# Kernel tuning notes

Hardware: AMD Instinct MI355X
Metric: run time of the kernel (lower is better)

Reference implementation:

```python
import jax, jax.numpy as jnp
import numpy as np

EMBED_DIM = 1024
B, S = 8, 2048


def setup_inputs() -> dict:
    key = jax.random.key(0)
    ks = jax.random.split(key, 8)
    scale = 1.0 / np.sqrt(EMBED_DIM)
    return {
        "mha_output": jax.random.normal(ks[0], (B, S, EMBED_DIM), dtype=jnp.float32),
        "gates": jax.random.uniform(ks[1], (B, S), dtype=jnp.float32),
        "Wq": jax.random.uniform(ks[2], (EMBED_DIM, EMBED_DIM), jnp.float32, -scale, scale),
        "bq": jax.random.uniform(ks[3], (EMBED_DIM,), jnp.float32, -scale, scale),
        "Wk": jax.random.uniform(ks[4], (EMBED_DIM, EMBED_DIM), jnp.float32, -scale, scale),
        "bk": jax.random.uniform(ks[5], (EMBED_DIM,), jnp.float32, -scale, scale),
        "Wv": jax.random.uniform(ks[6], (EMBED_DIM, EMBED_DIM), jnp.float32, -scale, scale),
        "bv": jax.random.uniform(ks[7], (EMBED_DIM,), jnp.float32, -scale, scale),
    }


def reference(mha_output, gates, Wq, bq, Wk, bk, Wv, bv):
    # gates: (B, S) -> (B, S, 1) for elementwise modulation
    g = gates[..., None]
    # Linear layers (torch convention: x @ W^T + b)
    Q = jnp.einsum('bsd,ed->bse', mha_output, Wq) + bq
    K = jnp.einsum('bsd,ed->bse', mha_output, Wk) + bk
    V = jnp.einsum('bsd,ed->bse', mha_output, Wv) + bv
    Q_mod = Q * g
    K_mod = K * g
    temperature = jnp.sqrt(jnp.asarray(EMBED_DIM, dtype=mha_output.dtype))
    scores = jnp.einsum('bqd,bkd->bqk', Q_mod, K_mod) / temperature  # (B, S, S)
    attn_weights = jax.nn.softmax(scores, axis=-1)
    gated_attn_output = jnp.einsum('bqk,bkd->bqd', attn_weights, V)
    return gated_attn_output, attn_weights
```

## Files before the change

kernel.cpp:

```cpp
#include <hip/hip_runtime.h>

#define SEQ  2048
#define EMB  1024
#define NBAT 8
#define NROW (NBAT*SEQ)

using u16 = unsigned short;
typedef float  f32x4  __attribute__((ext_vector_type(4)));
typedef __bf16 bf16x8 __attribute__((ext_vector_type(8)));
typedef u16    u16x8  __attribute__((ext_vector_type(8)));
typedef u16    u16x4  __attribute__((ext_vector_type(4)));

__device__ __forceinline__ u16 f2bf(float x) {
  unsigned u = __builtin_bit_cast(unsigned, x);
  return (u16)((u + 0x7fffu + ((u >> 16) & 1u)) >> 16);
}
__device__ __forceinline__ float bf2f(u16 h) {
  return __builtin_bit_cast(float, ((unsigned)h) << 16);
}

__device__ __forceinline__ f32x4 mfma16(u16x8 a, u16x8 b, f32x4 c) {
  return __builtin_amdgcn_mfma_f32_16x16x32_bf16(
      __builtin_bit_cast(bf16x8, a), __builtin_bit_cast(bf16x8, b), c, 0, 0, 0);
}

__device__ __forceinline__ void async_cp16(const u16* g, u16* l) {
  __builtin_amdgcn_global_load_lds(
      (const __attribute__((address_space(1))) void*)(g),
      (__attribute__((address_space(3))) void*)(l), 16, 0, 0);
}

__device__ __forceinline__ int xcd_swz(int bid, int nwg) {
  return (bid & 7) * (nwg >> 3) + (bid >> 3);
}

__device__ __forceinline__ void gload_tile128(const u16* __restrict__ g, int ld,
                                              u16* __restrict__ lds, int wid, int lane)
{
#pragma unroll
  for (int l = 0; l < 2; ++l) {
    const int r0 = wid * 32 + l * 16;
    const u16* src = g + (size_t)(r0 + (lane >> 2)) * ld + (lane & 3) * 8;
    async_cp16(src, lds + r0 * 32);
  }
}

__device__ __forceinline__ void kstep128(const u16* __restrict__ sA,
                                         const u16* __restrict__ sB,
                                         int wr, int wc, int lane, f32x4 acc[4][4])
{
  const int r = lane & 15, kg = lane >> 4;
  u16x8 a[4], b[4];
#pragma unroll
  for (int i = 0; i < 4; ++i) {
    a[i] = *(const u16x8*)&sA[(wr * 64 + i * 16 + r) * 32 + kg * 8];
    b[i] = *(const u16x8*)&sB[(wc * 64 + i * 16 + r) * 32 + kg * 8];
  }
#pragma unroll
  for (int i = 0; i < 4; ++i)
#pragma unroll
    for (int j = 0; j < 4; ++j)
      acc[i][j] = mfma16(a[i], b[j], acc[i][j]);
}

#define GEMM_PIPE3_128(Aptr, ldA, Bptr, ldB, NTv)                    \
  gload_tile128((Aptr), (ldA), sA0, wid, lane);                      \
  gload_tile128((Bptr), (ldB), sB0, wid, lane);                      \
  gload_tile128((Aptr) + 32, (ldA), sA1, wid, lane);                 \
  gload_tile128((Bptr) + 32, (ldB), sB1, wid, lane);                 \
  {                                                                  \
    u16 *pa0 = sA0, *pa1 = sA1, *pa2 = sA2;                          \
    u16 *pb0 = sB0, *pb1 = sB1, *pb2 = sB2;                          \
    for (int tt = 0; tt < (NTv) - 1; ++tt) {                         \
      asm volatile("s_waitcnt vmcnt(4)" ::: "memory");               \
      __builtin_amdgcn_s_barrier();                                  \
      __builtin_amdgcn_sched_barrier(0);                             \
      if (tt + 2 < (NTv)) {                                          \
        gload_tile128((Aptr) + (tt + 2) * 32, (ldA), pa2, wid, lane);\
        gload_tile128((Bptr) + (tt + 2) * 32, (ldB), pb2, wid, lane);\
      }                                                              \
      kstep128(pa0, pb0, wr, wc, lane, acc);                         \
      u16* tmp = pa0; pa0 = pa1; pa1 = pa2; pa2 = tmp;               \
      tmp = pb0; pb0 = pb1; pb1 = pb2; pb2 = tmp;                    \
    }                                                                \
    asm volatile("s_waitcnt vmcnt(0)" ::: "memory");                 \
    __builtin_amdgcn_s_barrier();                                    \
    __builtin_amdgcn_sched_barrier(0);                               \
    kstep128(pa0, pb0, wr, wc, lane, acc);                           \
  }

__device__ __forceinline__ void stage_half(const u16* __restrict__ g, int ld,
                                           u16* __restrict__ lds, int wid, int lane)
{
  const int lr = lane >> 2;
  const int bb = (lr & 1) ^ ((lr >> 2) & 1);
  const int row16 = (lr & ~1) | bb;
  const int ck = (lane & 3) ^ ((lr & 2) | bb);
#pragma unroll
  for (int l = 0; l < 2; ++l) {
    const int r0 = wid * 32 + l * 16;
    async_cp16(g + (size_t)(r0 + row16) * ld + ck * 8, lds + r0 * 32);
  }
}

__device__ __forceinline__ void ph_reads_A8(const u16* __restrict__ sAh,
                                            int wr, int r, int kg, int xr, u16x8 a[8])
{
#pragma unroll
  for (int i = 0; i < 8; ++i) {
    const int row = wr * 128 + i * 16 + r;
    a[i] = *(const u16x8*)&sAh[(row * 32 + kg * 8) ^ xr];
  }
}
__device__ __forceinline__ void ph_reads_B(const u16* __restrict__ sBh,
                                           int wc, int r, int kg, int xr, u16x8 b[4])
{
#pragma unroll
  for (int j = 0; j < 4; ++j) {
    const int row = wc * 64 + j * 16 + r;
    b[j] = *(const u16x8*)&sBh[(row * 32 + kg * 8) ^ xr];
  }
}

__device__ __forceinline__ void mfma_block8(const u16x8 a[8], const u16x8 b[4],
                                            f32x4 (*accp)[4])
{
#pragma unroll
  for (int i = 0; i < 8; ++i)
#pragma unroll
    for (int j = 0; j < 4; ++j)
      accp[i][j] = mfma16(a[i], b[j], accp[i][j]);
}

#define DECL_LDS_2PH()                                                       \
  __shared__ alignas(16) u16 sAls[2][2][256 * 32];                           \
  __shared__ alignas(16) u16 sBls[2][2][256 * 32]

#define PH2(READS, STAGE, WAIT)                                              \
  READS                                                                      \
  STAGE                                                                      \
  WAIT                                                                       \
  __builtin_amdgcn_s_barrier();                                              \
  asm volatile("s_waitcnt lgkmcnt(0)" ::: "memory");                         \
  __builtin_amdgcn_sched_barrier(0);                                         \
  __builtin_amdgcn_s_setprio(1);                                             \
  mfma_block8(a_, b_, acc);                                                  \
  __builtin_amdgcn_s_setprio(0);                                             \
  __builtin_amdgcn_s_barrier();

#define GEMM_2PH(Aptr, ldA, Bptr, ldB, NTv)                                  \
  {                                                                          \
    const int r_ = lane & 15, kg_ = lane >> 4;                               \
    const int xr_ = (r_ & 7) << 3;                                           \
    stage_half((Aptr),      (ldA), &sAls[0][0][0], wid, lane);               \
    stage_half((Aptr) + 32, (ldA), &sAls[0][1][0], wid, lane);               \
    stage_half((Bptr),      (ldB), &sBls[0][0][0], wid, lane);               \
    stage_half((Bptr) + 32, (ldB), &sBls[0][1][0], wid, lane);               \
    asm volatile("s_waitcnt vmcnt(2)" ::: "memory");                         \
    __builtin_amdgcn_sched_barrier(0);                                       \
    __builtin_amdgcn_s_barrier();                                            \
    u16x8 a_[8], b_[4];                                                      \
    for (int tt = 0; tt < (NTv); ++tt) {                                     \
      const int s_ = tt & 1, s2_ = s_ ^ 1;                                   \
      const u16* A0_ = &sAls[s_][0][0]; const u16* A1_ = &sAls[s_][1][0];    \
      const u16* B0_ = &sBls[s_][0][0]; const u16* B1_ = &sBls[s_][1][0];    \
      const bool pf_ = (tt + 1 < (NTv));                                     \
      PH2({ ph_reads_A8(A0_, wr, r_, kg_, xr_, a_);                          \
            ph_reads_B(B0_, wc, r_, kg_, xr_, b_); },                        \
          { if (pf_) {                                                       \
              stage_half((Aptr) + (tt + 1) * 64,      (ldA),                 \
                         &sAls[s2_][0][0], wid, lane);                       \
              stage_half((Aptr) + (tt + 1) * 64 + 32, (ldA),                 \
                         &sAls[s2_][1][0], wid, lane);                       \
              stage_half((Bptr) + (tt + 1) * 64,      (ldB),                 \
                         &sBls[s2_][0][0], wid, lane);                       \
              stage_half((Bptr) + (tt + 1) * 64 + 32, (ldB),                 \
                         &sBls[s2_][1][0], wid, lane);                       \
            } },                                                             \
          { if (pf_) asm volatile("s_waitcnt vmcnt(8)" ::: "memory");        \
            else     asm volatile("s_waitcnt vmcnt(0)" ::: "memory");        \
            __builtin_amdgcn_sched_barrier(0); })                            \
      PH2({ ph_reads_A8(A1_, wr, r_, kg_, xr_, a_);                          \
            ph_reads_B(B1_, wc, r_, kg_, xr_, b_); },                        \
          { },                                                               \
          { if (pf_) { asm volatile("s_waitcnt vmcnt(2)" ::: "memory");      \
            __builtin_amdgcn_sched_barrier(0); } })                          \
    }                                                                        \
  }

#define DECL_ACC84()                                                 \
  f32x4 acc[8][4];                                                   \
  _Pragma("unroll")                                                  \
  for (int i = 0; i < 8; ++i)                                        \
    _Pragma("unroll")                                                \
    for (int j = 0; j < 4; ++j)                                      \
      _Pragma("unroll")                                              \
      for (int q = 0; q < 4; ++q) acc[i][j][q] = 0.0f

__global__ __launch_bounds__(256) void prep_kernel(
    const float* __restrict__ X,
    const float* __restrict__ Wq, const float* __restrict__ Wk, const float* __restrict__ Wv,
    u16* __restrict__ Xb, u16* __restrict__ Wb)
{
  const size_t i = ((size_t)blockIdx.x * 256 + threadIdx.x) * 4;
  const size_t nx = (size_t)NROW * EMB;
  f32x4 v;
  u16* dst;
  if (i < nx) {
    v = *(const f32x4*)(X + i);
    dst = Xb + i;
  } else {
    const size_t j = i - nx;
    const int m = (int)(j / ((size_t)EMB * EMB));
    const size_t o = j - (size_t)m * EMB * EMB;
    const float* W = (m == 0) ? Wq : (m == 1) ? Wk : Wv;
    v = *(const f32x4*)(W + o);
    dst = Wb + j;
  }
  u16x4 h;
#pragma unroll
  for (int j = 0; j < 4; ++j) h[j] = f2bf(v[j]);
  *(u16x4*)dst = h;
}

__global__ __launch_bounds__(256) void proj_kernel(
    const u16* __restrict__ Xb, const u16* __restrict__ Wb,
    const float* __restrict__ bq, const float* __restrict__ bk, const float* __restrict__ bv,
    u16* __restrict__ Qb, u16* __restrict__ Kb, u16* __restrict__ VT)
{
  __shared__ alignas(16) u16 sA0[128 * 32], sA1[128 * 32], sA2[128 * 32];
  __shared__ alignas(16) u16 sB0[128 * 32], sB1[128 * 32], sB2[128 * 32];

  const int nwg = (EMB / 128) * (NROW / 128) * 3;
  int wg = xcd_swz(blockIdx.x, nwg);
  const int n0 = (wg & 7) * 128;        wg >>= 3;
  const int m0 = (wg & 127) * 128;      wg >>= 7;
  const int mat = wg;

  const int t = threadIdx.x, lane = t & 63, wid = t >> 6;
  const int wr = wid >> 1, wc = wid & 1;

  const u16* A = Xb + (size_t)m0 * EMB;
  const u16* B = Wb + (size_t)mat * EMB * EMB + (size_t)n0 * EMB;

  f32x4 acc[4][4];
#pragma unroll
  for (int i = 0; i < 4; ++i)
#pragma unroll
    for (int j = 0; j < 4; ++j)
#pragma unroll
      for (int q = 0; q < 4; ++q) acc[i][j][q] = 0.0f;

  GEMM_PIPE3_128(A, EMB, B, EMB, EMB / 32);

  const float* bias = (mat == 0) ? bq : (mat == 1) ? bk : bv;
  const int r = lane & 15, kg = lane >> 4;
#pragma unroll
  for (int i = 0; i < 4; ++i) {
#pragma unroll
    for (int j = 0; j < 4; ++j) {
      const int c = n0 + wc * 64 + j * 16 + r;
      const float bb = bias[c];
      if (mat == 2) {
        const int bi = m0 >> 11;
        const int sbase = (m0 & (SEQ - 1)) + wr * 64 + i * 16 + kg * 4;
        u16x4 hv;
#pragma unroll
        for (int rg = 0; rg < 4; ++rg) hv[rg] = f2bf(acc[i][j][rg] + bb);
        *(u16x4*)&VT[((size_t)bi * EMB + c) * SEQ + sbase] = hv;
      } else {
        u16* D = (mat == 0) ? Qb : Kb;
#pragma unroll
        for (int rg = 0; rg < 4; ++rg) {
          const int row = m0 + wr * 64 + i * 16 + kg * 4 + rg;
          D[(size_t)row * EMB + c] = f2bf(acc[i][j][rg] + bb);
        }
      }
    }
  }
}

__global__ __launch_bounds__(512, 2) void scores_kernel(
    const u16* __restrict__ Qb, const u16* __restrict__ Kb,
    const float* __restrict__ gates, u16* __restrict__ raw)
{
  DECL_LDS_2PH();
  const int nwg = 8 * 8 * NBAT;
  int wg = xcd_swz(blockIdx.x, nwg);
  const int n0 = (wg & 7) * 256;        wg >>= 3;
  const int q0 = (wg & 7) * 256;        wg >>= 3;
  const int b  = wg;

  const int t = threadIdx.x, lane = t & 63, wid = t >> 6;
  const int wr = wid >> 2, wc = wid & 3;

  const u16* A = Qb + ((size_t)b * SEQ + q0) * EMB;
  const u16* B = Kb + ((size_t)b * SEQ + n0) * EMB;

  DECL_ACC84();
  GEMM_2PH(A, EMB, B, EMB, EMB / 64);

  const float* gb = gates + (size_t)b * SEQ;
  u16* rawB = raw + ((size_t)b * SEQ + q0) * SEQ;
  const int r = lane & 15, kg = lane >> 4;

  float gkj[4];
#pragma unroll
  for (int j = 0; j < 4; ++j) gkj[j] = gb[n0 + wc * 64 + j * 16 + r] * 0.03125f;

#pragma unroll
  for (int i = 0; i < 8; ++i) {
#pragma unroll
    for (int rg = 0; rg < 4; ++rg) {
      const int qr = wr * 128 + i * 16 + kg * 4 + rg;
      const float gq = gb[q0 + qr];
#pragma unroll
      for (int j = 0; j < 4; ++j) {
        const int col = n0 + wc * 64 + j * 16 + r;
        rawB[(size_t)qr * SEQ + col] = f2bf(__expf(acc[i][j][rg] * gq * gkj[j]));
      }
    }
  }
}

__global__ __launch_bounds__(256) void rownorm_kernel(
    const u16* __restrict__ raw, float* __restrict__ attn, float* __restrict__ invl)
{
  const int row = blockIdx.x;
  const int t = threadIdx.x, lane = t & 63, wid = t >> 6;
  const u16* rp = raw + (size_t)row * SEQ + t * 8;
  u16x8 h = *(const u16x8*)rp;
  float e[8];
  float s = 0.f;
#pragma unroll
  for (int j = 0; j < 8; ++j) { e[j] = bf2f(h[j]); s += e[j]; }
#pragma unroll
  for (int off = 32; off >= 1; off >>= 1) s += __shfl_xor(s, off);
  __shared__ float red[4];
  if (lane == 0) red[wid] = s;
  __syncthreads();
  s = (red[0] + red[1]) + (red[2] + red[3]);
  const float iv = 1.0f / s;
  float* ap = attn + (size_t)row * SEQ + t * 8;
  f32x4 w0, w1;
#pragma unroll
  for (int j = 0; j < 4; ++j) { w0[j] = e[j] * iv; w1[j] = e[j + 4] * iv; }
  *(f32x4*)ap       = w0;
  *(f32x4*)(ap + 4) = w1;
  if (t == 0) invl[row] = iv;
}

__global__ __launch_bounds__(512, 2) void pv_kernel(
    const u16* __restrict__ Eb, const u16* __restrict__ VT,
    const float* __restrict__ invl, float* __restrict__ out)
{
  DECL_LDS_2PH();
  const int nwg = 4 * 8 * NBAT;
  int wg = xcd_swz(blockIdx.x, nwg);
  const int d0 = (wg & 3) * 256;        wg >>= 2;
  const int q0 = (wg & 7) * 256;        wg >>= 3;
  const int b  = wg;

  const int t = threadIdx.x, lane = t & 63, wid = t >> 6;
  const int wr = wid >> 2, wc = wid & 3;

  const u16* A = Eb + ((size_t)b * SEQ + q0) * SEQ;
  const u16* B = VT + ((size_t)b * EMB + d0) * SEQ;

  DECL_ACC84();
  GEMM_2PH(A, SEQ, B, SEQ, SEQ / 64);

  const int r = lane & 15, kg = lane >> 4;
#pragma unroll
  for (int i = 0; i < 8; ++i) {
#pragma unroll
    for (int rg = 0; rg < 4; ++rg) {
      const int rowl = q0 + wr * 128 + i * 16 + kg * 4 + rg;
      const float iv = invl[(size_t)b * SEQ + rowl];
#pragma unroll
      for (int j = 0; j < 4; ++j) {
        const int col = d0 + wc * 64 + j * 16 + r;
        out[((size_t)b * SEQ + rowl) * EMB + col] = acc[i][j][rg] * iv;
      }
    }
  }
}

extern "C" void kernel_launch(void* const* d_in, const int* in_sizes, int n_in,
                              void* d_out, int out_size, void* d_ws, size_t ws_size,
                              hipStream_t stream) {
  const float* X  = (const float*)d_in[0];
  const float* g  = (const float*)d_in[1];
  const float* Wq = (const float*)d_in[2];
  const float* bq = (const float*)d_in[3];
  const float* Wk = (const float*)d_in[4];
  const float* bk = (const float*)d_in[5];
  const float* Wv = (const float*)d_in[6];
  const float* bv = (const float*)d_in[7];

  float* out0 = (float*)d_out;
  float* attn = out0 + (size_t)NROW * EMB;

  const size_t rawN = (size_t)NBAT * SEQ * SEQ;
  const size_t need = rawN * 2 + (size_t)NBAT * EMB * SEQ * 2 + (size_t)NROW * 4;
  if (ws_size < need) return;
  u16* region0 = (u16*)d_ws;
  u16* Xb  = region0;
  u16* Wb  = region0 + (size_t)NROW * EMB;
  u16* raw = region0;
  u16* VT  = region0 + rawN;
  float* invl = (float*)(VT + (size_t)NBAT * EMB * SEQ);
  u16* Qb = (u16*)out0;
  u16* Kb = Qb + (size_t)NROW * EMB;

  const int prep_blocks = (int)(((size_t)NROW * EMB + (size_t)3 * EMB * EMB) / 1024);
  prep_kernel   <<<dim3(prep_blocks), 256, 0, stream>>>(X, Wq, Wk, Wv, Xb, Wb);
  proj_kernel   <<<dim3(3072), 256, 0, stream>>>(Xb, Wb, bq, bk, bv, Qb, Kb, VT);
  scores_kernel <<<dim3(512), 512, 0, stream>>>(Qb, Kb, g, raw);
  rownorm_kernel<<<dim3(NROW), 256, 0, stream>>>(raw, attn, invl);
  pv_kernel     <<<dim3(256), 512, 0, stream>>>(raw, VT, invl, out0);
}
```

Baseline: 354.2 us.

## Fuse softmax row normalization into scores and PV GEMM kernels

The scores kernel now computes per-tile partial row sums of the exponentiated bf16 scores and writes them to a workspace array. A tiny reduce kernel turns these into inverse row sums. The PV kernel writes the normalized fp32 attention weights straight from the LDS tiles it already stages for the GEMM, which removes the separate rownorm pass that re-read the raw score matrix. The staging order of A/B halves and the vmcnt waits were also reordered. This trades an extra full pass over the bf16 scores for extra global stores inside the PV GEMM loop, which may compete with its memory pipeline.

```diff
diff --git a/kernel.cpp b/kernel.cpp
--- a/kernel.cpp
+++ b/kernel.cpp
@@ -136,27 +136,15 @@
   __shared__ alignas(16) u16 sAls[2][2][256 * 32];                           \
   __shared__ alignas(16) u16 sBls[2][2][256 * 32]
 
-#define PH2(READS, STAGE, WAIT)                                              \
-  READS                                                                      \
-  STAGE                                                                      \
-  WAIT                                                                       \
-  __builtin_amdgcn_s_barrier();                                              \
-  asm volatile("s_waitcnt lgkmcnt(0)" ::: "memory");                         \
-  __builtin_amdgcn_sched_barrier(0);                                         \
-  __builtin_amdgcn_s_setprio(1);                                             \
-  mfma_block8(a_, b_, acc);                                                  \
-  __builtin_amdgcn_s_setprio(0);                                             \
-  __builtin_amdgcn_s_barrier();
-
-#define GEMM_2PH(Aptr, ldA, Bptr, ldB, NTv)                                  \
+#define GEMM_2PH(Aptr, ldA, Bptr, ldB, NTv, ...)                             \
   {                                                                          \
     const int r_ = lane & 15, kg_ = lane >> 4;                               \
     const int xr_ = (r_ & 7) << 3;                                           \
     stage_half((Aptr),      (ldA), &sAls[0][0][0], wid, lane);               \
+    stage_half((Bptr),      (ldB), &sBls[0][0][0], wid, lane);               \
     stage_half((Aptr) + 32, (ldA), &sAls[0][1][0], wid, lane);               \
-    stage_half((Bptr),      (ldB), &sBls[0][0][0], wid, lane);               \
     stage_half((Bptr) + 32, (ldB), &sBls[0][1][0], wid, lane);               \
-    asm volatile("s_waitcnt vmcnt(2)" ::: "memory");                         \
+    asm volatile("s_waitcnt vmcnt(4)" ::: "memory");                         \
     __builtin_amdgcn_sched_barrier(0);                                       \
     __builtin_amdgcn_s_barrier();                                            \
     u16x8 a_[8], b_[4];                                                      \
@@ -165,26 +153,35 @@
       const u16* A0_ = &sAls[s_][0][0]; const u16* A1_ = &sAls[s_][1][0];    \
       const u16* B0_ = &sBls[s_][0][0]; const u16* B1_ = &sBls[s_][1][0];    \
       const bool pf_ = (tt + 1 < (NTv));                                     \
-      PH2({ ph_reads_A8(A0_, wr, r_, kg_, xr_, a_);                          \
-            ph_reads_B(B0_, wc, r_, kg_, xr_, b_); },                        \
-          { if (pf_) {                                                       \
-              stage_half((Aptr) + (tt + 1) * 64,      (ldA),                 \
-                         &sAls[s2_][0][0], wid, lane);                       \
-              stage_half((Aptr) + (tt + 1) * 64 + 32, (ldA),                 \
-                         &sAls[s2_][1][0], wid, lane);                       \
-              stage_half((Bptr) + (tt + 1) * 64,      (ldB),                 \
-                         &sBls[s2_][0][0], wid, lane);                       \
-              stage_half((Bptr) + (tt + 1) * 64 + 32, (ldB),                 \
-                         &sBls[s2_][1][0], wid, lane);                       \
-            } },                                                             \
-          { if (pf_) asm volatile("s_waitcnt vmcnt(8)" ::: "memory");        \
-            else     asm volatile("s_waitcnt vmcnt(0)" ::: "memory");        \
-            __builtin_amdgcn_sched_barrier(0); })                            \
-      PH2({ ph_reads_A8(A1_, wr, r_, kg_, xr_, a_);                          \
-            ph_reads_B(B1_, wc, r_, kg_, xr_, b_); },                        \
-          { },                                                               \
-          { if (pf_) { asm volatile("s_waitcnt vmcnt(2)" ::: "memory");      \
-            __builtin_amdgcn_sched_barrier(0); } })                          \
+                                                           \
+      ph_reads_A8(A0_, wr, r_, kg_, xr_, a_);                                \
+      ph_reads_B(B0_, wc, r_, kg_, xr_, b_);                                 \
+      if (pf_) {                                                             \
+        stage_half((Aptr) + (tt + 1) * 64,      (ldA), &sAls[s2_][0][0], wid, lane); \
+        stage_half((Bptr) + (tt + 1) * 64,      (ldB), &sBls[s2_][0][0], wid, lane); \
+        stage_half((Aptr) + (tt + 1) * 64 + 32, (ldA), &sAls[s2_][1][0], wid, lane); \
+        stage_half((Bptr) + (tt + 1) * 64 + 32, (ldB), &sBls[s2_][1][0], wid, lane); \
+        asm volatile("s_waitcnt vmcnt(8)" ::: "memory");                     \
+      } else {                                                               \
+        asm volatile("s_waitcnt vmcnt(0)" ::: "memory");                     \
+      }                                                                      \
+      __builtin_amdgcn_sched_barrier(0);                                     \
+      __builtin_amdgcn_s_barrier();                                          \
+      __builtin_amdgcn_s_setprio(1);                                         \
+      mfma_block8(a_, b_, acc);                                              \
+      __builtin_amdgcn_s_setprio(0);                                         \
+      __builtin_amdgcn_s_barrier();                                          \
+                                                           \
+      ph_reads_A8(A1_, wr, r_, kg_, xr_, a_);                                \
+      ph_reads_B(B1_, wc, r_, kg_, xr_, b_);                                 \
+      __VA_ARGS__                                                            \
+      if (pf_) { asm volatile("s_waitcnt vmcnt(4)" ::: "memory");            \
+                 __builtin_amdgcn_sched_barrier(0); }                        \
+      __builtin_amdgcn_s_barrier();                                          \
+      __builtin_amdgcn_s_setprio(1);                                         \
+      mfma_block8(a_, b_, acc);                                              \
+      __builtin_amdgcn_s_setprio(0);                                         \
+      __builtin_amdgcn_s_barrier();                                          \
     }                                                                        \
   }
 
@@ -282,7 +279,8 @@
 
 __global__ __launch_bounds__(512, 2) void scores_kernel(
     const u16* __restrict__ Qb, const u16* __restrict__ Kb,
-    const float* __restrict__ gates, u16* __restrict__ raw)
+    const float* __restrict__ gates, u16* __restrict__ raw,
+    float* __restrict__ part)
 {
   DECL_LDS_2PH();
   const int nwg = 8 * 8 * NBAT;
@@ -298,11 +296,12 @@
   const u16* B = Kb + ((size_t)b * SEQ + n0) * EMB;
 
   DECL_ACC84();
-  GEMM_2PH(A, EMB, B, EMB, EMB / 64);
+  GEMM_2PH(A, EMB, B, EMB, EMB / 64, {});
 
   const float* gb = gates + (size_t)b * SEQ;
   u16* rawB = raw + ((size_t)b * SEQ + q0) * SEQ;
   const int r = lane & 15, kg = lane >> 4;
+  const int tix = (n0 >> 6) + wc;
 
   float gkj[4];
 #pragma unroll
@@ -314,50 +313,45 @@
     for (int rg = 0; rg < 4; ++rg) {
       const int qr = wr * 128 + i * 16 + kg * 4 + rg;
       const float gq = gb[q0 + qr];
+      float psum = 0.f;
 #pragma unroll
       for (int j = 0; j < 4; ++j) {
         const int col = n0 + wc * 64 + j * 16 + r;
-        rawB[(size_t)qr * SEQ + col] = f2bf(__expf(acc[i][j][rg] * gq * gkj[j]));
+        const u16 h = f2bf(__expf(acc[i][j][rg] * gq * gkj[j]));
+        rawB[(size_t)qr * SEQ + col] = h;
+        psum += bf2f(h);
       }
+#pragma unroll
+      for (int m = 1; m < 16; m <<= 1) psum += __shfl_xor(psum, m);
+      if (r == 0) part[((size_t)b * SEQ + q0 + qr) * 32 + tix] = psum;
     }
   }
 }
 
-__global__ __launch_bounds__(256) void rownorm_kernel(
-    const u16* __restrict__ raw, float* __restrict__ attn, float* __restrict__ invl)
-{
-  const int row = blockIdx.x;
-  const int t = threadIdx.x, lane = t & 63, wid = t >> 6;
-  const u16* rp = raw + (size_t)row * SEQ + t * 8;
-  u16x8 h = *(const u16x8*)rp;
-  float e[8];
+__global__ __launch_bounds__(256) void reduce_kernel(
+    const float* __restrict__ part, float* __restrict__ invl)
+{
+  const int row = blockIdx.x * 256 + threadIdx.x;
+  const float* p = part + (size_t)row * 32;
   float s = 0.f;
 #pragma unroll
-  for (int j = 0; j < 8; ++j) { e[j] = bf2f(h[j]); s += e[j]; }
-#pragma unroll
-  for (int off = 32; off >= 1; off >>= 1) s += __shfl_xor(s, off);
-  __shared__ float red[4];
-  if (lane == 0) red[wid] = s;
-  __syncthreads();
-  s = (red[0] + red[1]) + (red[2] + red[3]);
-  const float iv = 1.0f / s;
-  float* ap = attn + (size_t)row * SEQ + t * 8;
-  f32x4 w0, w1;
-#pragma unroll
-  for (int j = 0; j < 4; ++j) { w0[j] = e[j] * iv; w1[j] = e[j + 4] * iv; }
-  *(f32x4*)ap       = w0;
-  *(f32x4*)(ap + 4) = w1;
-  if (t == 0) invl[row] = iv;
+  for (int i = 0; i < 8; ++i) {
+    f32x4 v = *(const f32x4*)(p + i * 4);
+    s += (v[0] + v[1]) + (v[2] + v[3]);
+  }
+  invl[row] = 1.0f / s;
 }
 
 __global__ __launch_bounds__(512, 2) void pv_kernel(
     const u16* __restrict__ Eb, const u16* __restrict__ VT,
-    const float* __restrict__ invl, float* __restrict__ out)
+    const float* __restrict__ invl, float* __restrict__ attn,
+    float* __restrict__ out)
 {
   DECL_LDS_2PH();
   const int nwg = 4 * 8 * NBAT;
   int wg = xcd_swz(blockIdx.x, nwg);
-  const int d0 = (wg & 3) * 256;        wg >>= 2;
+  const int dd = wg & 3;                wg >>= 2;
+  const int d0 = dd * 256;
   const int q0 = (wg & 7) * 256;        wg >>= 3;
   const int b  = wg;
 
@@ -367,8 +361,25 @@
   const u16* A = Eb + ((size_t)b * SEQ + q0) * SEQ;
   const u16* B = VT + ((size_t)b * EMB + d0) * SEQ;
 
+  const int prow = t >> 1, pc2 = t & 1;
+  const float invl_r = invl[(size_t)b * SEQ + q0 + prow];
+  float* attnB = attn + ((size_t)b * SEQ + q0) * SEQ;
+
   DECL_ACC84();
-  GEMM_2PH(A, SEQ, B, SEQ, SEQ / 64);
+  GEMM_2PH(A, SEQ, B, SEQ, SEQ / 64,
+    {
+      const u16* hb_ = (dd >= 2) ? A1_ : A0_;
+      const int ch_ = (dd & 1) * 2 + pc2;
+      u16x8 hv_ = *(const u16x8*)&hb_[(prow * 32 + ch_ * 8) ^ ((prow & 7) << 3)];
+      f32x4 w0_, w1_;
+      w0_[0] = bf2f(hv_[0]) * invl_r;  w0_[1] = bf2f(hv_[1]) * invl_r;
+      w0_[2] = bf2f(hv_[2]) * invl_r;  w0_[3] = bf2f(hv_[3]) * invl_r;
+      w1_[0] = bf2f(hv_[4]) * invl_r;  w1_[1] = bf2f(hv_[5]) * invl_r;
+      w1_[2] = bf2f(hv_[6]) * invl_r;  w1_[3] = bf2f(hv_[7]) * invl_r;
+      float* ap_ = attnB + (size_t)prow * SEQ + tt * 64 + dd * 16 + pc2 * 8;
+      *(f32x4*)ap_ = w0_;
+      *(f32x4*)(ap_ + 4) = w1_;
+    });
 
   const int r = lane & 15, kg = lane >> 4;
 #pragma unroll
@@ -402,21 +413,23 @@
   float* attn = out0 + (size_t)NROW * EMB;
 
   const size_t rawN = (size_t)NBAT * SEQ * SEQ;
-  const size_t need = rawN * 2 + (size_t)NBAT * EMB * SEQ * 2 + (size_t)NROW * 4;
+  const size_t need = rawN * 2 + (size_t)NBAT * EMB * SEQ * 2
+                    + (size_t)NROW * 32 * 4 + (size_t)NROW * 4;
   if (ws_size < need) return;
   u16* region0 = (u16*)d_ws;
   u16* Xb  = region0;
   u16* Wb  = region0 + (size_t)NROW * EMB;
   u16* raw = region0;
   u16* VT  = region0 + rawN;
-  float* invl = (float*)(VT + (size_t)NBAT * EMB * SEQ);
+  float* part = (float*)(VT + (size_t)NBAT * EMB * SEQ);
+  float* invl = part + (size_t)NROW * 32;
   u16* Qb = (u16*)out0;
   u16* Kb = Qb + (size_t)NROW * EMB;
 
   const int prep_blocks = (int)(((size_t)NROW * EMB + (size_t)3 * EMB * EMB) / 1024);
   prep_kernel   <<<dim3(prep_blocks), 256, 0, stream>>>(X, Wq, Wk, Wv, Xb, Wb);
   proj_kernel   <<<dim3(3072), 256, 0, stream>>>(Xb, Wb, bq, bk, bv, Qb, Kb, VT);
-  scores_kernel <<<dim3(512), 512, 0, stream>>>(Qb, Kb, g, raw);
-  rownorm_kernel<<<dim3(NROW), 256, 0, stream>>>(raw, attn, invl);
-  pv_kernel     <<<dim3(256), 512, 0, stream>>>(raw, VT, invl, out0);
-}
+  scores_kernel <<<dim3(512), 512, 0, stream>>>(Qb, Kb, g, raw, part);
+  reduce_kernel <<<dim3(NROW / 256), 256, 0, stream>>>(part, invl);
+  pv_kernel     <<<dim3(256), 512, 0, stream>>>(raw, VT, invl, attn, out0);
+}
```

Result: no change. 353.4 us (-0.2%).
